# Performance work log

Measured on AMD Instinct MI355X. Metric: run time of the kernel, lower is better.

Reference implementation:

```python
import jax, jax.numpy as jnp
import numpy as np

H = 256; NH = 8; DH = H // NH; L = 2; B = 32; S = 512; FIN = 199; A = 4


def _ln(x, g, b):
    m = jnp.mean(x, -1, keepdims=True)
    v = jnp.mean((x - m) ** 2, -1, keepdims=True)
    return (x - m) / jnp.sqrt(v + 1e-5) * g + b


def _grn(x, fc1w, fc1b, fc2w, fc2b, gw, gb, ggw, ggb, lg, lb):
    # GatedResidualNetwork, input_dim == output_dim so no skip layer, no context
    h = jax.nn.elu(x @ fc1w + fc1b)
    h = jax.nn.elu(h @ fc2w + fc2b)
    g = (h @ gw + gb) * jax.nn.sigmoid(h @ ggw + ggb)  # GLU
    return _ln(g + x, lg, lb)


def _attn(h, wq, bq, wk, bk, wv, bv, wo, bo):
    b, s, _ = h.shape
    q = (h @ wq + bq).reshape(b, s, NH, DH)
    k = (h @ wk + bk).reshape(b, s, NH, DH)
    v = (h @ wv + bv).reshape(b, s, NH, DH)
    scores = jnp.einsum('bqhd,bkhd->bhqk', q, k) / jnp.sqrt(jnp.float32(DH))
    mask = jnp.triu(jnp.ones((s, s), dtype=bool), 1)  # causal: mask strictly-future
    scores = jnp.where(mask, -jnp.inf, scores)
    aw = jax.nn.softmax(scores, axis=-1)
    ctx = jnp.einsum('bhqk,bkhd->bqhd', aw, v).reshape(b, s, H)
    return ctx @ wo + bo, aw


def _pe(s, d):
    pos = jnp.arange(s, dtype=jnp.float32)[:, None]
    div = jnp.exp(jnp.arange(0, d, 2, dtype=jnp.float32) * (-jnp.log(10000.0) / d))
    pe = jnp.zeros((s, d), dtype=jnp.float32)
    pe = pe.at[:, 0::2].set(jnp.sin(pos * div)).at[:, 1::2].set(jnp.cos(pos * div))
    return pe


def setup_inputs():
    key = jax.random.key(0)
    ks = iter(jax.random.split(key, 80))
    def nrm(shape, sc=0.02):
        return (jax.random.normal(next(ks), shape) * sc).astype(jnp.float32)
    d = {}
    d['x'] = jax.random.normal(next(ks), (B, S, FIN), dtype=jnp.float32)
    d['time_features'] = jax.random.normal(next(ks), (B, S, 3), dtype=jnp.float32)
    d['fp_w'] = nrm((FIN, H)); d['fp_b'] = jnp.zeros((H,), jnp.float32)
    d['tp_w'] = nrm((3, H));   d['tp_b'] = jnp.zeros((H,), jnp.float32)
    d['ip_w'] = nrm((H, H));   d['ip_b'] = jnp.zeros((H,), jnp.float32)
    for nm in ['wq', 'wk', 'wv', 'wo']:
        d[nm] = nrm((L, H, H))
    for nm in ['bq', 'bk', 'bv', 'bo']:
        d[nm] = jnp.zeros((L, H), jnp.float32)
    d['ln_g'] = jnp.ones((L, H), jnp.float32); d['ln_b'] = jnp.zeros((L, H), jnp.float32)
    for nm in ['g_fc1w', 'g_fc2w', 'g_gw', 'g_ggw']:
        d[nm] = nrm((L, H, H))
    for nm in ['g_fc1b', 'g_fc2b', 'g_gb', 'g_ggb']:
        d[nm] = jnp.zeros((L, H), jnp.float32)
    d['g_lg'] = jnp.ones((L, H), jnp.float32); d['g_lb'] = jnp.zeros((L, H), jnp.float32)
    for nm in ['f_fc1w', 'f_fc2w', 'f_gw', 'f_ggw']:
        d[nm] = nrm((H, H))
    for nm in ['f_fc1b', 'f_fc2b', 'f_gb', 'f_ggb']:
        d[nm] = jnp.zeros((H,), jnp.float32)
    d['f_lg'] = jnp.ones((H,), jnp.float32); d['f_lb'] = jnp.zeros((H,), jnp.float32)
    d['out_w'] = nrm((H, A)); d['out_b'] = jnp.zeros((A,), jnp.float32)
    return d


def reference(x, time_features, fp_w, fp_b, tp_w, tp_b, ip_w, ip_b,
              wq, bq, wk, bk, wv, bv, wo, bo, ln_g, ln_b,
              g_fc1w, g_fc1b, g_fc2w, g_fc2b, g_gw, g_gb, g_ggw, g_ggb, g_lg, g_lb,
              f_fc1w, f_fc1b, f_fc2w, f_fc2b, f_gw, f_gb, f_ggw, f_ggb, f_lg, f_lb,
              out_w, out_b):
    s = x.shape[1]
    hidden = (x @ fp_w + fp_b) + (time_features @ tp_w + tp_b)
    hidden = hidden @ ip_w + ip_b
    hidden = hidden + _pe(s, H)[None]
    aw = None
    for i in range(L):
        ao, aw = _attn(hidden, wq[i], bq[i], wk[i], bk[i], wv[i], bv[i], wo[i], bo[i])
        hidden = _ln(hidden + ao, ln_g[i], ln_b[i])
        hidden = _grn(hidden, g_fc1w[i], g_fc1b[i], g_fc2w[i], g_fc2b[i],
                      g_gw[i], g_gb[i], g_ggw[i], g_ggb[i], g_lg[i], g_lb[i])
    hidden = _grn(hidden, f_fc1w, f_fc1b, f_fc2w, f_fc2b, f_gw, f_gb, f_ggw, f_ggb, f_lg, f_lb)
    final = hidden[:, -1, :]
    logits = final @ out_w + out_b  # [B, A], one column per target asset
    return (logits, aw)
```

## Files before the change

kernel.cpp:

```cpp
#include <hip/hip_runtime.h>
#include <math.h>
#include <cstddef>

#define H 256
#define NH 8
#define DH 32
#define LAYERS 2
#define BB 32
#define SS 512
#define FINDIM 199
#define AA 4
#define T_TOK (BB*SS)

typedef unsigned short u16;
typedef unsigned int u32;
typedef __attribute__((ext_vector_type(8))) short short8;
typedef __attribute__((ext_vector_type(4))) float f4;

__device__ __forceinline__ float b2f(u16 v){
  unsigned u = ((unsigned)v) << 16;
  return __builtin_bit_cast(float, u);
}
__device__ __forceinline__ u16 f2b(float f){
  unsigned u = __builtin_bit_cast(unsigned, f);
  unsigned r = (u + 0x7fffu + ((u >> 16) & 1u)) >> 16;
  return (u16)r;
}
__device__ __forceinline__ float wave_sum(float v){
  #pragma unroll
  for (int mk=1; mk<64; mk<<=1) v += __shfl_xor(v, mk, 64);
  return v;
}

#define GLD_LDS16(g, l) \
  __builtin_amdgcn_global_load_lds((const __attribute__((address_space(1))) void*)(g), \
                                   (__attribute__((address_space(3))) void*)(l), 16, 0, 0)

struct WPtrs { const float* p[21]; };

__global__ __launch_bounds__(256) void wconv_kernel(WPtrs wp, u16* __restrict__ dst){
  __shared__ float tl[64][65];
  int mb = blockIdx.x >> 4, tile = blockIdx.x & 15;
  int k0 = (tile >> 2) * 64, n0 = (tile & 3) * 64;
  const float* src = wp.p[mb];
  int t = threadIdx.x;
  int r = t >> 4, cg = t & 15;
  #pragma unroll
  for (int p4=0;p4<4;p4++){
    f4 v = *(const f4*)(src + (size_t)(k0 + r + p4*16)*H + n0 + cg*4);
    tl[r+p4*16][cg*4+0]=v[0]; tl[r+p4*16][cg*4+1]=v[1];
    tl[r+p4*16][cg*4+2]=v[2]; tl[r+p4*16][cg*4+3]=v[3];
  }
  __syncthreads();
  u16* db = dst + (size_t)mb*H*H;
  #pragma unroll
  for (int p4=0;p4<4;p4++){
    int rn = r + p4*16;
    ushort4 o;
    o.x = f2b(tl[cg*4+0][rn]); o.y = f2b(tl[cg*4+1][rn]);
    o.z = f2b(tl[cg*4+2][rn]); o.w = f2b(tl[cg*4+3][rn]);
    *(ushort4*)(db + (size_t)(n0+rn)*H + k0 + cg*4) = o;
  }
}

__global__ __launch_bounds__(256) void in_proj_kernel(
    const float* __restrict__ x, const float* __restrict__ tf,
    const float* __restrict__ fp_w, const float* __restrict__ fp_b,
    const float* __restrict__ tp_w, const float* __restrict__ tp_b,
    u16* __restrict__ out) {
  __shared__ float xs[8][FINDIM];
  __shared__ float ts[8][3];
  int t = threadIdx.x;
  int tok0 = blockIdx.x * 8;
  for (int idx = t; idx < 8*FINDIM; idx += 256) {
    int r = idx / FINDIM, k = idx % FINDIM;
    xs[r][k] = x[(size_t)(tok0+r)*FINDIM + k];
  }
  if (t < 24) { int r = t/3, k = t%3; ts[r][k] = tf[(size_t)(tok0+r)*3 + k]; }
  __syncthreads();
  int c = t;
  float base = fp_b[c] + tp_b[c];
  float acc[8];
  #pragma unroll
  for (int r=0;r<8;r++) acc[r] = base;
  for (int k=0;k<FINDIM;k++){
    float w = fp_w[k*H + c];
    #pragma unroll
    for (int r=0;r<8;r++) acc[r] = fmaf(xs[r][k], w, acc[r]);
  }
  #pragma unroll
  for (int k=0;k<3;k++){
    float w = tp_w[k*H + c];
    #pragma unroll
    for (int r=0;r<8;r++) acc[r] = fmaf(ts[r][k], w, acc[r]);
  }
  #pragma unroll
  for (int r=0;r<8;r++) out[(size_t)(tok0+r)*H + c] = f2b(acc[r]);
}

struct GemmJob  { const u16* Wt; const float* bias; u16* C; };
struct GemmBatch{ GemmJob j[3]; };

template<int EPI>
__global__ __launch_bounds__(256) void gemm_bf16(
    const u16* __restrict__ A, GemmBatch jb) {
  __shared__ u16 smem[128*64 + 64*64];
  u16* As  = smem;
  u16* Wsm = smem + 128*64;
  const GemmJob job = jb.j[blockIdx.z];
  const u16* Wt = job.Wt;
  int t = threadIdx.x;
  int m0 = blockIdx.x * 128;
  int n0 = blockIdx.y * 64;
  int lane = t & 63, w = t >> 6;
  int wr = (w >> 1) * 64;
  int wc = (w & 1) * 32;
  int l16 = lane & 15, lq = lane >> 4;

  f4 acc[4][2];
  #pragma unroll
  for (int mi=0;mi<4;mi++)
    #pragma unroll
    for (int ni=0;ni<2;ni++) acc[mi][ni] = (f4){0.f,0.f,0.f,0.f};

  for (int k0=0;k0<256;k0+=64){
    #pragma unroll
    for (int ja=0;ja<4;ja++){
      int ub = (w*4 + ja)*64;
      int u  = ub + lane;
      int m  = u >> 3, c = u & 7, kx = c ^ (m & 7);
      const u16* g = A + (size_t)(m0+m)*H + k0 + kx*8;
      GLD_LDS16(g, As + (size_t)ub*8);
    }
    #pragma unroll
    for (int jb2=0;jb2<2;jb2++){
      int ub = (w*2 + jb2)*64;
      int u  = ub + lane;
      int n  = u >> 3, c = u & 7, kx = c ^ (n & 7);
      const u16* g = Wt + (size_t)(n0+n)*H + k0 + kx*8;
      GLD_LDS16(g, Wsm + (size_t)ub*8);
    }
    __syncthreads();
    #pragma unroll
    for (int kc=0;kc<2;kc++){
      short8 af[4], bf[2];
      int kx = kc*4 + lq;
      #pragma unroll
      for (int mi=0;mi<4;mi++){
        int m = wr + mi*16 + l16;
        int un = (m<<3) | (kx ^ (m&7));
        af[mi] = *(short8*)&As[un*8];
      }
      #pragma unroll
      for (int ni=0;ni<2;ni++){
        int n = wc + ni*16 + l16;
        int un = (n<<3) | (kx ^ (n&7));
        bf[ni] = *(short8*)&Wsm[un*8];
      }
      #pragma unroll
      for (int mi=0;mi<4;mi++)
        #pragma unroll
        for (int ni=0;ni<2;ni++)
          acc[mi][ni] = __builtin_amdgcn_mfma_f32_16x16x32_bf16(af[mi], bf[ni], acc[mi][ni], 0,0,0);
    }
    __syncthreads();
  }

  u16* Cl = smem;
  #pragma unroll
  for (int ni=0;ni<2;ni++){
    int coll = wc + ni*16 + l16;
    float bcol = job.bias[n0 + coll];
    #pragma unroll
    for (int mi=0;mi<4;mi++){
      #pragma unroll
      for (int r=0;r<4;r++){
        int rowl = wr + mi*16 + lq*4 + r;
        float v = acc[mi][ni][r] + bcol;
        if (EPI==1) v = v > 0.f ? v : expm1f(v);
        if (EPI==2) {
          int s  = (m0 + rowl) & (SS-1);
          int ii = (n0 + coll) >> 1;
          float div = __expf((float)(2*ii) * -0.03597789207803197f);
          float arg = (float)s * div;
          v += ((n0+coll) & 1) ? cosf(arg) : sinf(arg);
        }
        Cl[rowl*68 + coll] = f2b(v);
      }
    }
  }
  __syncthreads();
  #pragma unroll
  for (int q2=0;q2<4;q2++){
    int u = q2*256 + t;
    int row = u >> 3, cu = u & 7;
    short8 val = *(short8*)&Cl[row*68 + cu*8];
    *(short8*)(job.C + (size_t)(m0+row)*H + n0 + cu*8) = val;
  }
}

template<int WRITE_AW>
__global__ __launch_bounds__(256) void attn_kernel(
    const u16* __restrict__ q, const u16* __restrict__ k,
    const u16* __restrict__ v, float* __restrict__ aw,
    u16* __restrict__ ctx) {
  __shared__ u16 Vt[DH][SS+8];
  __shared__ u16 Plds[4][16][72];
  int t  = threadIdx.x;
  int zg = blockIdx.x;
  int bh = blockIdx.y;
  int b  = bh >> 3, h = bh & 7;
  int lane = t & 63, w = t >> 6;
  int l16 = lane & 15, lq = lane >> 4;
  const float scale = 0.17677669529663687f;

  #pragma unroll
  for (int rep=0;rep<2;rep++){
    int kk = t + rep*256;
    const u16* vp = v + ((size_t)(b*SS + kk))*H + h*DH;
    short8 r0 = *(const short8*)(vp);
    short8 r1 = *(const short8*)(vp+8);
    short8 r2 = *(const short8*)(vp+16);
    short8 r3 = *(const short8*)(vp+24);
    #pragma unroll
    for (int j=0;j<8;j++){
      Vt[j][kk]    = (u16)r0[j];
      Vt[8+j][kk]  = (u16)r1[j];
      Vt[16+j][kk] = (u16)r2[j];
      Vt[24+j][kk] = (u16)r3[j];
    }
  }
  __syncthreads();

  for (int it=0; it<4; it++){
    int qt  = zg + it*2;
    int qr0 = qt*64 + w*16;
    int KT  = qt*4 + w + 1;
    short8 af = *(const short8*)(q + ((size_t)(b*SS + qr0 + l16))*H + h*DH + lq*8);

    float l[4] = {0.f,0.f,0.f,0.f};
    f4 o[2] = {(f4){0.f,0.f,0.f,0.f}, (f4){0.f,0.f,0.f,0.f}};
    u32 pk0[32], pk1[32];

    #pragma unroll
    for (int c8=0;c8<8;c8++){
      if (c8*4 < KT){
        #pragma unroll
        for (int j=0;j<4;j++){
          int kt = c8*4 + j;
          float p[4] = {0.f,0.f,0.f,0.f};
          if (kt < KT){
            short8 bfr = *(const short8*)(k + ((size_t)(b*SS + kt*16 + l16))*H + h*DH + lq*8);
            f4 cc = (f4){0.f,0.f,0.f,0.f};
            cc = __builtin_amdgcn_mfma_f32_16x16x32_bf16(af, bfr, cc, 0,0,0);
            int col = kt*16 + l16;
            #pragma unroll
            for (int i=0;i<4;i++){
              int qi = qr0 + lq*4 + i;
              float sc = (col <= qi) ? cc[i]*scale : -3.0e38f;
              p[i] = __expf(sc);
              l[i] += p[i];
            }
          }
          u16 pb[4];
          #pragma unroll
          for (int i=0;i<4;i++) pb[i] = f2b(p[i]);
          if (WRITE_AW){
            pk0[kt] = (u32)pb[0] | ((u32)pb[1] << 16);
            pk1[kt] = (u32)pb[2] | ((u32)pb[3] << 16);
          }
          #pragma unroll
          for (int i=0;i<4;i++) Plds[w][lq*4+i][j*16+l16] = pb[i];
        }
        #pragma unroll
        for (int kc=0;kc<2;kc++){
          short8 pa = *(short8*)&Plds[w][l16][kc*32 + lq*8];
          #pragma unroll
          for (int dt=0;dt<2;dt++){
            short8 vb = *(const short8*)&Vt[dt*16 + l16][c8*64 + kc*32 + lq*8];
            o[dt] = __builtin_amdgcn_mfma_f32_16x16x32_bf16(pa, vb, o[dt], 0,0,0);
          }
        }
      }
    }

    #pragma unroll
    for (int i=0;i<4;i++){
      #pragma unroll
      for (int mk=1; mk<16; mk<<=1) l[i] += __shfl_xor(l[i], mk, 64);
    }
    float inv[4];
    #pragma unroll
    for (int i=0;i<4;i++) inv[i] = 1.0f / l[i];

    if (WRITE_AW){
      float* ab = aw + (size_t)bh*SS*SS;
      #pragma unroll
      for (int kt=0;kt<32;kt++){
        if (kt < KT){
          int col = kt*16 + l16;
          float pv[4] = { b2f((u16)pk0[kt]), b2f((u16)(pk0[kt]>>16)),
                          b2f((u16)pk1[kt]), b2f((u16)(pk1[kt]>>16)) };
          #pragma unroll
          for (int i=0;i<4;i++){
            int qi = qr0 + lq*4 + i;
            ab[(size_t)qi*SS + col] = (col <= qi) ? pv[i]*inv[i] : 0.f;
          }
        }
      }
      int c4base = KT*4;
      f4 z = (f4){0.f,0.f,0.f,0.f};
      #pragma unroll
      for (int ri=0;ri<4;ri++){
        int row = qr0 + ri*4 + lq;
        for (int j=l16; j < 128 - c4base; j += 16)
          *(f4*)&ab[(size_t)row*SS + (size_t)(c4base+j)*4] = z;
      }
    }

    #pragma unroll
    for (int dt=0;dt<2;dt++){
      #pragma unroll
      for (int i=0;i<4;i++){
        int row = qr0 + lq*4 + i;
        ctx[((size_t)(b*SS + row))*H + h*DH + dt*16 + l16] = f2b(o[dt][i]*inv[i]);
      }
    }
  }
}

__global__ __launch_bounds__(256) void add_ln_kernel(
    u16* __restrict__ hid, const u16* __restrict__ ao,
    const float* __restrict__ g, const float* __restrict__ b){
  int wv = threadIdx.x>>6, lane = threadIdx.x&63;
  size_t tok = (size_t)blockIdx.x*4 + wv;
  u16* hp = hid + tok*H + lane*4;
  ushort4 h4 = *(ushort4*)hp;
  ushort4 a4 = *(const ushort4*)(ao + tok*H + lane*4);
  float xv[4] = {b2f(h4.x)+b2f(a4.x), b2f(h4.y)+b2f(a4.y),
                 b2f(h4.z)+b2f(a4.z), b2f(h4.w)+b2f(a4.w)};
  float s=0.f, ss=0.f;
  #pragma unroll
  for (int j=0;j<4;j++){ s += xv[j]; ss += xv[j]*xv[j]; }
  s = wave_sum(s); ss = wave_sum(ss);
  float mean = s * (1.0f/H);
  float var  = ss * (1.0f/H) - mean*mean;
  float rstd = rsqrtf(var + 1e-5f);
  ushort4 o;
  int col = lane*4;
  o.x = f2b((xv[0]-mean)*rstd*g[col+0] + b[col+0]);
  o.y = f2b((xv[1]-mean)*rstd*g[col+1] + b[col+1]);
  o.z = f2b((xv[2]-mean)*rstd*g[col+2] + b[col+2]);
  o.w = f2b((xv[3]-mean)*rstd*g[col+3] + b[col+3]);
  *(ushort4*)hp = o;
}

__global__ __launch_bounds__(256) void gate_ln_kernel(
    const u16* __restrict__ gbuf, const u16* __restrict__ ggbuf,
    u16* __restrict__ hid,
    const float* __restrict__ lg, const float* __restrict__ lb){
  int wv = threadIdx.x>>6, lane = threadIdx.x&63;
  size_t tok = (size_t)blockIdx.x*4 + wv;
  u16* hp = hid + tok*H + lane*4;
  ushort4 g4  = *(const ushort4*)(gbuf  + tok*H + lane*4);
  ushort4 gg4 = *(const ushort4*)(ggbuf + tok*H + lane*4);
  ushort4 h4  = *(ushort4*)hp;
  float gv[4]  = {b2f(g4.x),  b2f(g4.y),  b2f(g4.z),  b2f(g4.w)};
  float ggv[4] = {b2f(gg4.x), b2f(gg4.y), b2f(gg4.z), b2f(gg4.w)};
  float hv[4]  = {b2f(h4.x),  b2f(h4.y),  b2f(h4.z),  b2f(h4.w)};
  float xv[4];
  #pragma unroll
  for (int j=0;j<4;j++){
    float sg = 1.0f/(1.0f + __expf(-ggv[j]));
    xv[j] = gv[j]*sg + hv[j];
  }
  float s=0.f, ss=0.f;
  #pragma unroll
  for (int j=0;j<4;j++){ s += xv[j]; ss += xv[j]*xv[j]; }
  s = wave_sum(s); ss = wave_sum(ss);
  float mean = s * (1.0f/H);
  float var  = ss * (1.0f/H) - mean*mean;
  float rstd = rsqrtf(var + 1e-5f);
  ushort4 o;
  int col = lane*4;
  o.x = f2b((xv[0]-mean)*rstd*lg[col+0] + lb[col+0]);
  o.y = f2b((xv[1]-mean)*rstd*lg[col+1] + lb[col+1]);
  o.z = f2b((xv[2]-mean)*rstd*lg[col+2] + lb[col+2]);
  o.w = f2b((xv[3]-mean)*rstd*lg[col+3] + lb[col+3]);
  *(ushort4*)hp = o;
}

__global__ __launch_bounds__(128) void logits_kernel(
    const u16* __restrict__ hid, const float* __restrict__ ow,
    const float* __restrict__ ob, float* __restrict__ out){
  int t = threadIdx.x;
  int b = t >> 2, a = t & 3;
  const u16* hr = hid + ((size_t)b*SS + (SS-1))*H;
  float acc = ob[a];
  for (int k2=0;k2<H;k2++) acc = fmaf(b2f(hr[k2]), ow[k2*AA + a], acc);
  out[t] = acc;
}

extern "C" void kernel_launch(void* const* d_in, const int* in_sizes, int n_in,
                              void* d_out, int out_size, void* d_ws, size_t ws_size,
                              hipStream_t stream){
  (void)in_sizes; (void)n_in; (void)out_size; (void)ws_size;
  const float* x      = (const float*)d_in[0];
  const float* tf     = (const float*)d_in[1];
  const float* fp_w   = (const float*)d_in[2];
  const float* fp_b   = (const float*)d_in[3];
  const float* tp_w   = (const float*)d_in[4];
  const float* tp_b   = (const float*)d_in[5];
  const float* ip_w   = (const float*)d_in[6];
  const float* ip_b   = (const float*)d_in[7];
  const float* wq     = (const float*)d_in[8];
  const float* wk     = (const float*)d_in[9];
  const float* wv     = (const float*)d_in[10];
  const float* wo     = (const float*)d_in[11];
  const float* bq     = (const float*)d_in[12];
  const float* bk     = (const float*)d_in[13];
  const float* bv     = (const float*)d_in[14];
  const float* bo     = (const float*)d_in[15];
  const float* ln_g   = (const float*)d_in[16];
  const float* ln_b   = (const float*)d_in[17];
  const float* g_fc1w = (const float*)d_in[18];
  const float* g_fc2w = (const float*)d_in[19];
  const float* g_gw   = (const float*)d_in[20];
  const float* g_ggw  = (const float*)d_in[21];
  const float* g_fc1b = (const float*)d_in[22];
  const float* g_fc2b = (const float*)d_in[23];
  const float* g_gb   = (const float*)d_in[24];
  const float* g_ggb  = (const float*)d_in[25];
  const float* g_lg   = (const float*)d_in[26];
  const float* g_lb   = (const float*)d_in[27];
  const float* f_fc1w = (const float*)d_in[28];
  const float* f_fc2w = (const float*)d_in[29];
  const float* f_gw   = (const float*)d_in[30];
  const float* f_ggw  = (const float*)d_in[31];
  const float* f_fc1b = (const float*)d_in[32];
  const float* f_fc2b = (const float*)d_in[33];
  const float* f_gb   = (const float*)d_in[34];
  const float* f_ggb  = (const float*)d_in[35];
  const float* f_lg   = (const float*)d_in[36];
  const float* f_lb   = (const float*)d_in[37];
  const float* out_w  = (const float*)d_in[38];
  const float* out_b  = (const float*)d_in[39];

  float* logits = (float*)d_out;
  float* aw     = logits + BB*AA;

  u16* wts = (u16*)d_ws;
  const size_t WMAT = (size_t)H*H;
  u16* hid  = wts  + 21*WMAT;
  size_t BUF = (size_t)T_TOK * H;
  u16* buf1 = hid  + BUF;
  u16* buf2 = buf1 + BUF;
  u16* buf3 = buf2 + BUF;

  WPtrs wp;
  wp.p[0]  = ip_w;
  wp.p[1]  = wq;        wp.p[2]  = wq + WMAT;
  wp.p[3]  = wk;        wp.p[4]  = wk + WMAT;
  wp.p[5]  = wv;        wp.p[6]  = wv + WMAT;
  wp.p[7]  = wo;        wp.p[8]  = wo + WMAT;
  wp.p[9]  = g_fc1w;    wp.p[10] = g_fc1w + WMAT;
  wp.p[11] = g_fc2w;    wp.p[12] = g_fc2w + WMAT;
  wp.p[13] = g_gw;      wp.p[14] = g_gw + WMAT;
  wp.p[15] = g_ggw;     wp.p[16] = g_ggw + WMAT;
  wp.p[17] = f_fc1w;    wp.p[18] = f_fc2w;
  wp.p[19] = f_gw;      wp.p[20] = f_ggw;
  const int WT_IP=0, WT_Q=1, WT_K=3, WT_V=5, WT_O=7,
            WT_FC1=9, WT_FC2=11, WT_GW=13, WT_GGW=15,
            WT_FFC1=17, WT_FFC2=18, WT_FGW=19, WT_FGGW=20;

  dim3 b256(256);
  dim3 gAttn(2, BB*NH);

  auto mkbatch = [&](int w0, const float* b0, u16* c0,
                     int w1, const float* b1, u16* c1,
                     int w2, const float* b2, u16* c2) {
    GemmBatch gb;
    gb.j[0] = { wts + (size_t)w0*WMAT, b0, c0 };
    gb.j[1] = { wts + (size_t)(w1<0?w0:w1)*WMAT, (w1<0?b0:b1), (w1<0?c0:c1) };
    gb.j[2] = { wts + (size_t)(w2<0?w0:w2)*WMAT, (w2<0?b0:b2), (w2<0?c0:c2) };
    return gb;
  };

  wconv_kernel<<<21*16, b256, 0, stream>>>(wp, wts);
  in_proj_kernel<<<T_TOK/8, b256, 0, stream>>>(x, tf, fp_w, fp_b, tp_w, tp_b, buf1);

  gemm_bf16<2><<<dim3(T_TOK/128, H/64, 1), b256, 0, stream>>>(
      buf1, mkbatch(WT_IP, ip_b, hid, -1,0,0, -1,0,0));

  for (int i=0;i<LAYERS;i++){
    const size_t BOFF = (size_t)i*H;
    gemm_bf16<0><<<dim3(T_TOK/128, H/64, 3), b256, 0, stream>>>(
        hid, mkbatch(WT_Q+i, bq+BOFF, buf1, WT_K+i, bk+BOFF, buf2, WT_V+i, bv+BOFF, buf3));
    if (i == LAYERS-1)
      attn_kernel<1><<<gAttn, b256, 0, stream>>>(buf1, buf2, buf3, aw, buf1);
    else
      attn_kernel<0><<<gAttn, b256, 0, stream>>>(buf1, buf2, buf3, aw, buf1);
    gemm_bf16<0><<<dim3(T_TOK/128, H/64, 1), b256, 0, stream>>>(
        buf1, mkbatch(WT_O+i, bo+BOFF, buf2, -1,0,0, -1,0,0));
    add_ln_kernel<<<T_TOK/4, b256, 0, stream>>>(hid, buf2, ln_g + BOFF, ln_b + BOFF);
    gemm_bf16<1><<<dim3(T_TOK/128, H/64, 1), b256, 0, stream>>>(
        hid, mkbatch(WT_FC1+i, g_fc1b+BOFF, buf1, -1,0,0, -1,0,0));
    gemm_bf16<1><<<dim3(T_TOK/128, H/64, 1), b256, 0, stream>>>(
        buf1, mkbatch(WT_FC2+i, g_fc2b+BOFF, buf2, -1,0,0, -1,0,0));
    gemm_bf16<0><<<dim3(T_TOK/128, H/64, 2), b256, 0, stream>>>(
        buf2, mkbatch(WT_GW+i, g_gb+BOFF, buf3, WT_GGW+i, g_ggb+BOFF, buf1, -1,0,0));
    gate_ln_kernel<<<T_TOK/4, b256, 0, stream>>>(buf3, buf1, hid, g_lg + BOFF, g_lb + BOFF);
  }

  gemm_bf16<1><<<dim3(T_TOK/128, H/64, 1), b256, 0, stream>>>(
      hid, mkbatch(WT_FFC1, f_fc1b, buf1, -1,0,0, -1,0,0));
  gemm_bf16<1><<<dim3(T_TOK/128, H/64, 1), b256, 0, stream>>>(
      buf1, mkbatch(WT_FFC2, f_fc2b, buf2, -1,0,0, -1,0,0));
  gemm_bf16<0><<<dim3(T_TOK/128, H/64, 2), b256, 0, stream>>>(
      buf2, mkbatch(WT_FGW, f_gb, buf3, WT_FGGW, f_ggb, buf1, -1,0,0));
  gate_ln_kernel<<<T_TOK/4, b256, 0, stream>>>(buf3, buf1, hid, f_lg, f_lb);

  logits_kernel<<<1, 128, 0, stream>>>(hid, out_w, out_b, logits);
}
```

Baseline: 748.5 us.

## Fuse GRN, O-projection+LN and input projection into per-token-tile MFMA kernels

Replaces the chain of separate GEMM and layernorm kernels with fused kernels. Each block holds a 32-token tile in LDS and runs the successive 256x256 matmuls with MFMA, keeping intermediates on chip: the O-projection with residual and layernorm, the whole GRN (fc1, fc2, GLU, residual, LN), and the input projection done as a bf16 MFMA GEMM over padded concatenated features followed by ip_w and positional encoding. This removes several global round-trips of the activation buffers and many launches. In exchange, B fragments are read straight from global memory (L2) without LDS staging or double buffering, there are only 512 blocks, and an extra padded bf16 copy of the input is materialised.

```diff
diff --git a/kernel.cpp b/kernel.cpp
--- a/kernel.cpp
+++ b/kernel.cpp
@@ -11,6 +11,7 @@
 #define FINDIM 199
 #define AA 4
 #define T_TOK (BB*SS)
+#define KIN 224
 
 typedef unsigned short u16;
 typedef unsigned int u32;
@@ -35,6 +36,89 @@
 #define GLD_LDS16(g, l) \
   __builtin_amdgcn_global_load_lds((const __attribute__((address_space(1))) void*)(g), \
                                    (__attribute__((address_space(3))) void*)(l), 16, 0, 0)
+
+template<int KC, int WK>
+__device__ __forceinline__ void stage_acc(
+    const u16* Xl, int sx, const u16* __restrict__ Wt,
+    int c0, int l16, int lq, f4 acc[2][2])
+{
+  #pragma unroll
+  for (int mi=0;mi<2;mi++)
+    #pragma unroll
+    for (int ni=0;ni<2;ni++) acc[mi][ni] = (f4){0.f,0.f,0.f,0.f};
+  #pragma unroll
+  for (int kc=0;kc<KC;kc++){
+    short8 af[2], bf[2];
+    af[0] = *(const short8*)&Xl[(l16)*sx      + kc*32 + lq*8];
+    af[1] = *(const short8*)&Xl[(16+l16)*sx   + kc*32 + lq*8];
+    bf[0] = *(const short8*)(Wt + (size_t)(c0+l16)*WK    + kc*32 + lq*8);
+    bf[1] = *(const short8*)(Wt + (size_t)(c0+16+l16)*WK + kc*32 + lq*8);
+    #pragma unroll
+    for (int mi=0;mi<2;mi++)
+      #pragma unroll
+      for (int ni=0;ni<2;ni++)
+        acc[mi][ni] = __builtin_amdgcn_mfma_f32_16x16x32_bf16(af[mi], bf[ni], acc[mi][ni], 0,0,0);
+  }
+}
+
+template<int DO_ELU>
+__device__ __forceinline__ void stage_store(
+    f4 acc[2][2], const float* __restrict__ bias,
+    int c0, int l16, int lq, u16* Yl, int sy)
+{
+  #pragma unroll
+  for (int ni=0;ni<2;ni++){
+    int col = c0 + ni*16 + l16;
+    float bc = bias[col];
+    #pragma unroll
+    for (int mi=0;mi<2;mi++){
+      #pragma unroll
+      for (int r=0;r<4;r++){
+        int row = mi*16 + lq*4 + r;
+        float v = acc[mi][ni][r] + bc;
+        if (DO_ELU) v = v > 0.f ? v : expm1f(v);
+        Yl[row*sy + col] = f2b(v);
+      }
+    }
+  }
+}
+
+__device__ __forceinline__ void tile_load256(const u16* g, u16* Yl, int sy, int t){
+  #pragma unroll
+  for (int j=0;j<2;j++){
+    int u = t + j*512;
+    int row = u >> 5, cu = u & 31;
+    *(short8*)&Yl[row*sy + cu*8] = *(const short8*)(g + (size_t)row*H + cu*8);
+  }
+}
+
+__device__ __forceinline__ void tile_ln(
+    const u16* Yl, int sy, const float* __restrict__ g, const float* __restrict__ b,
+    u16* out, int t)
+{
+  int w = t >> 6, lane = t & 63;
+  #pragma unroll
+  for (int rr=0;rr<4;rr++){
+    int row = w*4 + rr;
+    float xv[4];
+    #pragma unroll
+    for (int j=0;j<4;j++) xv[j] = b2f(Yl[row*sy + lane*4 + j]);
+    float s=0.f, ss=0.f;
+    #pragma unroll
+    for (int j=0;j<4;j++){ s += xv[j]; ss += xv[j]*xv[j]; }
+    s = wave_sum(s); ss = wave_sum(ss);
+    float mean = s * (1.0f/H);
+    float var  = ss * (1.0f/H) - mean*mean;
+    float rstd = rsqrtf(var + 1e-5f);
+    ushort4 o;
+    int col = lane*4;
+    o.x = f2b((xv[0]-mean)*rstd*g[col+0] + b[col+0]);
+    o.y = f2b((xv[1]-mean)*rstd*g[col+1] + b[col+1]);
+    o.z = f2b((xv[2]-mean)*rstd*g[col+2] + b[col+2]);
+    o.w = f2b((xv[3]-mean)*rstd*g[col+3] + b[col+3]);
+    *(ushort4*)(out + (size_t)row*H + col) = o;
+  }
+}
 
 struct WPtrs { const float* p[21]; };
 
@@ -63,45 +147,183 @@
   }
 }
 
-__global__ __launch_bounds__(256) void in_proj_kernel(
+__global__ __launch_bounds__(256) void wcat_kernel(
+    const float* __restrict__ fp_w, const float* __restrict__ tp_w,
+    u16* __restrict__ wcat){
+  int idx = blockIdx.x*256 + threadIdx.x;
+  if (idx >= 256*KIN) return;
+  int n = idx / KIN, k2 = idx % KIN;
+  float v = 0.f;
+  if (k2 < FINDIM) v = fp_w[(size_t)k2*H + n];
+  else if (k2 < FINDIM+3) v = tp_w[(size_t)(k2-FINDIM)*H + n];
+  wcat[idx] = f2b(v);
+}
+
+__global__ __launch_bounds__(256) void xconv_kernel(
     const float* __restrict__ x, const float* __restrict__ tf,
-    const float* __restrict__ fp_w, const float* __restrict__ fp_b,
-    const float* __restrict__ tp_w, const float* __restrict__ tp_b,
-    u16* __restrict__ out) {
-  __shared__ float xs[8][FINDIM];
-  __shared__ float ts[8][3];
+    u16* __restrict__ ab){
+  size_t idx = (size_t)blockIdx.x*256 + threadIdx.x;
+  if (idx >= (size_t)T_TOK*KIN) return;
+  int tok = idx / KIN, k2 = idx % KIN;
+  float v = 0.f;
+  if (k2 < FINDIM) v = x[(size_t)tok*FINDIM + k2];
+  else if (k2 < FINDIM+3) v = tf[(size_t)tok*3 + (k2-FINDIM)];
+  ab[idx] = f2b(v);
+}
+
+#define SA (KIN+8)
+#define SY (H+8)
+
+__global__ __launch_bounds__(512) void input_kernel(
+    const u16* __restrict__ ab, const u16* __restrict__ wcat,
+    const float* __restrict__ fp_b, const float* __restrict__ tp_b,
+    const u16* __restrict__ ipw, const float* __restrict__ ip_b,
+    u16* __restrict__ hid){
+  __shared__ u16 Al[32*SA];
+  __shared__ u16 Tl[32*SY];
   int t = threadIdx.x;
-  int tok0 = blockIdx.x * 8;
-  for (int idx = t; idx < 8*FINDIM; idx += 256) {
-    int r = idx / FINDIM, k = idx % FINDIM;
-    xs[r][k] = x[(size_t)(tok0+r)*FINDIM + k];
-  }
-  if (t < 24) { int r = t/3, k = t%3; ts[r][k] = tf[(size_t)(tok0+r)*3 + k]; }
-  __syncthreads();
-  int c = t;
-  float base = fp_b[c] + tp_b[c];
-  float acc[8];
-  #pragma unroll
-  for (int r=0;r<8;r++) acc[r] = base;
-  for (int k=0;k<FINDIM;k++){
-    float w = fp_w[k*H + c];
-    #pragma unroll
-    for (int r=0;r<8;r++) acc[r] = fmaf(xs[r][k], w, acc[r]);
-  }
-  #pragma unroll
-  for (int k=0;k<3;k++){
-    float w = tp_w[k*H + c];
-    #pragma unroll
-    for (int r=0;r<8;r++) acc[r] = fmaf(ts[r][k], w, acc[r]);
-  }
-  #pragma unroll
-  for (int r=0;r<8;r++) out[(size_t)(tok0+r)*H + c] = f2b(acc[r]);
+  int tok0 = blockIdx.x * 32;
+  int lane = t & 63, w = t >> 6;
+  int l16 = lane & 15, lq = lane >> 4;
+  int c0 = w * 32;
+
+  #pragma unroll
+  for (int j=0;j<2;j++){
+    int u = t + j*512;
+    if (u < 896){
+      int row = u / 28, cu = u % 28;
+      *(short8*)&Al[row*SA + cu*8] = *(const short8*)(ab + (size_t)(tok0+row)*KIN + cu*8);
+    }
+  }
+  __syncthreads();
+
+  f4 acc[2][2];
+  stage_acc<7, KIN>(Al, SA, wcat, c0, l16, lq, acc);
+  #pragma unroll
+  for (int ni=0;ni<2;ni++){
+    int col = c0 + ni*16 + l16;
+    float bc = fp_b[col] + tp_b[col];
+    #pragma unroll
+    for (int mi=0;mi<2;mi++)
+      #pragma unroll
+      for (int r=0;r<4;r++){
+        int row = mi*16 + lq*4 + r;
+        Tl[row*SY + col] = f2b(acc[mi][ni][r] + bc);
+      }
+  }
+  __syncthreads();
+
+  stage_acc<8, H>(Tl, SY, ipw, c0, l16, lq, acc);
+  #pragma unroll
+  for (int ni=0;ni<2;ni++){
+    int col = c0 + ni*16 + l16;
+    float bc = ip_b[col];
+    int ii = col >> 1;
+    float div = __expf((float)(2*ii) * -0.03597789207803197f);
+    #pragma unroll
+    for (int mi=0;mi<2;mi++)
+      #pragma unroll
+      for (int r=0;r<4;r++){
+        int row = mi*16 + lq*4 + r;
+        int s = (tok0 + row) & (SS-1);
+        float arg = (float)s * div;
+        float pe = (col & 1) ? cosf(arg) : sinf(arg);
+        hid[(size_t)(tok0+row)*H + col] = f2b(acc[mi][ni][r] + bc + pe);
+      }
+  }
+}
+
+__global__ __launch_bounds__(512) void oproj_ln_kernel(
+    const u16* __restrict__ ctx, u16* __restrict__ hid,
+    const u16* __restrict__ wo, const float* __restrict__ bo,
+    const float* __restrict__ g, const float* __restrict__ b){
+  __shared__ u16 Xl[32*SY];
+  __shared__ u16 Rl[32*SY];
+  int t = threadIdx.x;
+  int tok0 = blockIdx.x * 32;
+  int lane = t & 63, w = t >> 6;
+  int l16 = lane & 15, lq = lane >> 4;
+  int c0 = w * 32;
+  u16* hb = hid + (size_t)tok0*H;
+
+  tile_load256(ctx + (size_t)tok0*H, Xl, SY, t);
+  tile_load256(hb, Rl, SY, t);
+  __syncthreads();
+
+  f4 acc[2][2];
+  stage_acc<8, H>(Xl, SY, wo, c0, l16, lq, acc);
+  __syncthreads();
+  #pragma unroll
+  for (int ni=0;ni<2;ni++){
+    int col = c0 + ni*16 + l16;
+    float bc = bo[col];
+    #pragma unroll
+    for (int mi=0;mi<2;mi++)
+      #pragma unroll
+      for (int r=0;r<4;r++){
+        int row = mi*16 + lq*4 + r;
+        float y = acc[mi][ni][r] + bc + b2f(Rl[row*SY + col]);
+        Xl[row*SY + col] = f2b(y);
+      }
+  }
+  __syncthreads();
+  tile_ln(Xl, SY, g, b, hb, t);
+}
+
+__global__ __launch_bounds__(512) void grn_kernel(
+    u16* __restrict__ hid,
+    const u16* __restrict__ fc1, const u16* __restrict__ fc2,
+    const u16* __restrict__ gw,  const u16* __restrict__ ggw,
+    const float* __restrict__ b1, const float* __restrict__ b2,
+    const float* __restrict__ gb, const float* __restrict__ ggb,
+    const float* __restrict__ lg, const float* __restrict__ lb){
+  __shared__ u16 Xl[32*SY];
+  __shared__ u16 H1[32*SY];
+  __shared__ u16 H2[32*SY];
+  int t = threadIdx.x;
+  int tok0 = blockIdx.x * 32;
+  int lane = t & 63, w = t >> 6;
+  int l16 = lane & 15, lq = lane >> 4;
+  int c0 = w * 32;
+  u16* hb = hid + (size_t)tok0*H;
+
+  tile_load256(hb, Xl, SY, t);
+  __syncthreads();
+
+  f4 acc[2][2];
+  stage_acc<8, H>(Xl, SY, fc1, c0, l16, lq, acc);
+  stage_store<1>(acc, b1, c0, l16, lq, H1, SY);
+  __syncthreads();
+  stage_acc<8, H>(H1, SY, fc2, c0, l16, lq, acc);
+  stage_store<1>(acc, b2, c0, l16, lq, H2, SY);
+  __syncthreads();
+  stage_acc<8, H>(H2, SY, gw, c0, l16, lq, acc);
+  stage_store<0>(acc, gb, c0, l16, lq, H1, SY);
+  __syncthreads();
+  stage_acc<8, H>(H2, SY, ggw, c0, l16, lq, acc);
+  __syncthreads();
+  #pragma unroll
+  for (int ni=0;ni<2;ni++){
+    int col = c0 + ni*16 + l16;
+    float bc = ggb[col];
+    #pragma unroll
+    for (int mi=0;mi<2;mi++)
+      #pragma unroll
+      for (int r=0;r<4;r++){
+        int row = mi*16 + lq*4 + r;
+        float gg = acc[mi][ni][r] + bc;
+        float sg = 1.0f/(1.0f + __expf(-gg));
+        float y  = b2f(H1[row*SY + col]) * sg + b2f(Xl[row*SY + col]);
+        H2[row*SY + col] = f2b(y);
+      }
+  }
+  __syncthreads();
+  tile_ln(H2, SY, lg, lb, hb, t);
 }
 
 struct GemmJob  { const u16* Wt; const float* bias; u16* C; };
 struct GemmBatch{ GemmJob j[3]; };
 
-template<int EPI>
 __global__ __launch_bounds__(256) void gemm_bf16(
     const u16* __restrict__ A, GemmBatch jb) {
   __shared__ u16 smem[128*64 + 64*64];
@@ -176,16 +398,7 @@
       #pragma unroll
       for (int r=0;r<4;r++){
         int rowl = wr + mi*16 + lq*4 + r;
-        float v = acc[mi][ni][r] + bcol;
-        if (EPI==1) v = v > 0.f ? v : expm1f(v);
-        if (EPI==2) {
-          int s  = (m0 + rowl) & (SS-1);
-          int ii = (n0 + coll) >> 1;
-          float div = __expf((float)(2*ii) * -0.03597789207803197f);
-          float arg = (float)s * div;
-          v += ((n0+coll) & 1) ? cosf(arg) : sinf(arg);
-        }
-        Cl[rowl*68 + coll] = f2b(v);
+        Cl[rowl*68 + coll] = f2b(acc[mi][ni][r] + bcol);
       }
     }
   }
@@ -327,67 +540,6 @@
       }
     }
   }
-}
-
-__global__ __launch_bounds__(256) void add_ln_kernel(
-    u16* __restrict__ hid, const u16* __restrict__ ao,
-    const float* __restrict__ g, const float* __restrict__ b){
-  int wv = threadIdx.x>>6, lane = threadIdx.x&63;
-  size_t tok = (size_t)blockIdx.x*4 + wv;
-  u16* hp = hid + tok*H + lane*4;
-  ushort4 h4 = *(ushort4*)hp;
-  ushort4 a4 = *(const ushort4*)(ao + tok*H + lane*4);
-  float xv[4] = {b2f(h4.x)+b2f(a4.x), b2f(h4.y)+b2f(a4.y),
-                 b2f(h4.z)+b2f(a4.z), b2f(h4.w)+b2f(a4.w)};
-  float s=0.f, ss=0.f;
-  #pragma unroll
-  for (int j=0;j<4;j++){ s += xv[j]; ss += xv[j]*xv[j]; }
-  s = wave_sum(s); ss = wave_sum(ss);
-  float mean = s * (1.0f/H);
-  float var  = ss * (1.0f/H) - mean*mean;
-  float rstd = rsqrtf(var + 1e-5f);
-  ushort4 o;
-  int col = lane*4;
-  o.x = f2b((xv[0]-mean)*rstd*g[col+0] + b[col+0]);
-  o.y = f2b((xv[1]-mean)*rstd*g[col+1] + b[col+1]);
-  o.z = f2b((xv[2]-mean)*rstd*g[col+2] + b[col+2]);
-  o.w = f2b((xv[3]-mean)*rstd*g[col+3] + b[col+3]);
-  *(ushort4*)hp = o;
-}
-
-__global__ __launch_bounds__(256) void gate_ln_kernel(
-    const u16* __restrict__ gbuf, const u16* __restrict__ ggbuf,
-    u16* __restrict__ hid,
-    const float* __restrict__ lg, const float* __restrict__ lb){
-  int wv = threadIdx.x>>6, lane = threadIdx.x&63;
-  size_t tok = (size_t)blockIdx.x*4 + wv;
-  u16* hp = hid + tok*H + lane*4;
-  ushort4 g4  = *(const ushort4*)(gbuf  + tok*H + lane*4);
-  ushort4 gg4 = *(const ushort4*)(ggbuf + tok*H + lane*4);
-  ushort4 h4  = *(ushort4*)hp;
-  float gv[4]  = {b2f(g4.x),  b2f(g4.y),  b2f(g4.z),  b2f(g4.w)};
-  float ggv[4] = {b2f(gg4.x), b2f(gg4.y), b2f(gg4.z), b2f(gg4.w)};
-  float hv[4]  = {b2f(h4.x),  b2f(h4.y),  b2f(h4.z),  b2f(h4.w)};
-  float xv[4];
-  #pragma unroll
-  for (int j=0;j<4;j++){
-    float sg = 1.0f/(1.0f + __expf(-ggv[j]));
-    xv[j] = gv[j]*sg + hv[j];
-  }
-  float s=0.f, ss=0.f;
-  #pragma unroll
-  for (int j=0;j<4;j++){ s += xv[j]; ss += xv[j]*xv[j]; }
-  s = wave_sum(s); ss = wave_sum(ss);
-  float mean = s * (1.0f/H);
-  float var  = ss * (1.0f/H) - mean*mean;
-  float rstd = rsqrtf(var + 1e-5f);
-  ushort4 o;
-  int col = lane*4;
-  o.x = f2b((xv[0]-mean)*rstd*lg[col+0] + lb[col+0]);
-  o.y = f2b((xv[1]-mean)*rstd*lg[col+1] + lb[col+1]);
-  o.z = f2b((xv[2]-mean)*rstd*lg[col+2] + lb[col+2]);
-  o.w = f2b((xv[3]-mean)*rstd*lg[col+3] + lb[col+3]);
-  *(ushort4*)hp = o;
 }
 
 __global__ __launch_bounds__(128) void logits_kernel(
@@ -451,7 +603,9 @@
 
   u16* wts = (u16*)d_ws;
   const size_t WMAT = (size_t)H*H;
-  u16* hid  = wts  + 21*WMAT;
+  u16* wcat = wts  + 21*WMAT;
+  u16* abuf = wcat + (size_t)H*KIN;
+  u16* hid  = abuf + (size_t)T_TOK*KIN;
   size_t BUF = (size_t)T_TOK * H;
   u16* buf1 = hid  + BUF;
   u16* buf2 = buf1 + BUF;
@@ -473,52 +627,40 @@
             WT_FC1=9, WT_FC2=11, WT_GW=13, WT_GGW=15,
             WT_FFC1=17, WT_FFC2=18, WT_FGW=19, WT_FGGW=20;
 
-  dim3 b256(256);
+  dim3 b256(256), b512(512);
   dim3 gAttn(2, BB*NH);
-
-  auto mkbatch = [&](int w0, const float* b0, u16* c0,
-                     int w1, const float* b1, u16* c1,
-                     int w2, const float* b2, u16* c2) {
-    GemmBatch gb;
-    gb.j[0] = { wts + (size_t)w0*WMAT, b0, c0 };
-    gb.j[1] = { wts + (size_t)(w1<0?w0:w1)*WMAT, (w1<0?b0:b1), (w1<0?c0:c1) };
-    gb.j[2] = { wts + (size_t)(w2<0?w0:w2)*WMAT, (w2<0?b0:b2), (w2<0?c0:c2) };
-    return gb;
-  };
+  dim3 gTok(T_TOK/32);
 
   wconv_kernel<<<21*16, b256, 0, stream>>>(wp, wts);
-  in_proj_kernel<<<T_TOK/8, b256, 0, stream>>>(x, tf, fp_w, fp_b, tp_w, tp_b, buf1);
-
-  gemm_bf16<2><<<dim3(T_TOK/128, H/64, 1), b256, 0, stream>>>(
-      buf1, mkbatch(WT_IP, ip_b, hid, -1,0,0, -1,0,0));
+  wcat_kernel<<<(H*KIN+255)/256, b256, 0, stream>>>(fp_w, tp_w, wcat);
+  xconv_kernel<<<(T_TOK*KIN+255)/256, b256, 0, stream>>>(x, tf, abuf);
+  input_kernel<<<gTok, b512, 0, stream>>>(abuf, wcat, fp_b, tp_b,
+                                          wts + (size_t)WT_IP*WMAT, ip_b, hid);
 
   for (int i=0;i<LAYERS;i++){
     const size_t BOFF = (size_t)i*H;
-    gemm_bf16<0><<<dim3(T_TOK/128, H/64, 3), b256, 0, stream>>>(
-        hid, mkbatch(WT_Q+i, bq+BOFF, buf1, WT_K+i, bk+BOFF, buf2, WT_V+i, bv+BOFF, buf3));
+    GemmBatch gb;
+    gb.j[0] = { wts + (size_t)(WT_Q+i)*WMAT, bq+BOFF, buf1 };
+    gb.j[1] = { wts + (size_t)(WT_K+i)*WMAT, bk+BOFF, buf2 };
+    gb.j[2] = { wts + (size_t)(WT_V+i)*WMAT, bv+BOFF, buf3 };
+    gemm_bf16<<<dim3(T_TOK/128, H/64, 3), b256, 0, stream>>>(hid, gb);
     if (i == LAYERS-1)
       attn_kernel<1><<<gAttn, b256, 0, stream>>>(buf1, buf2, buf3, aw, buf1);
     else
       attn_kernel<0><<<gAttn, b256, 0, stream>>>(buf1, buf2, buf3, aw, buf1);
-    gemm_bf16<0><<<dim3(T_TOK/128, H/64, 1), b256, 0, stream>>>(
-        buf1, mkbatch(WT_O+i, bo+BOFF, buf2, -1,0,0, -1,0,0));
-    add_ln_kernel<<<T_TOK/4, b256, 0, stream>>>(hid, buf2, ln_g + BOFF, ln_b + BOFF);
-    gemm_bf16<1><<<dim3(T_TOK/128, H/64, 1), b256, 0, stream>>>(
-        hid, mkbatch(WT_FC1+i, g_fc1b+BOFF, buf1, -1,0,0, -1,0,0));
-    gemm_bf16<1><<<dim3(T_TOK/128, H/64, 1), b256, 0, stream>>>(
-        buf1, mkbatch(WT_FC2+i, g_fc2b+BOFF, buf2, -1,0,0, -1,0,0));
-    gemm_bf16<0><<<dim3(T_TOK/128, H/64, 2), b256, 0, stream>>>(
-        buf2, mkbatch(WT_GW+i, g_gb+BOFF, buf3, WT_GGW+i, g_ggb+BOFF, buf1, -1,0,0));
-    gate_ln_kernel<<<T_TOK/4, b256, 0, stream>>>(buf3, buf1, hid, g_lg + BOFF, g_lb + BOFF);
-  }
-
-  gemm_bf16<1><<<dim3(T_TOK/128, H/64, 1), b256, 0, stream>>>(
-      hid, mkbatch(WT_FFC1, f_fc1b, buf1, -1,0,0, -1,0,0));
-  gemm_bf16<1><<<dim3(T_TOK/128, H/64, 1), b256, 0, stream>>>(
-      buf1, mkbatch(WT_FFC2, f_fc2b, buf2, -1,0,0, -1,0,0));
-  gemm_bf16<0><<<dim3(T_TOK/128, H/64, 2), b256, 0, stream>>>(
-      buf2, mkbatch(WT_FGW, f_gb, buf3, WT_FGGW, f_ggb, buf1, -1,0,0));
-  gate_ln_kernel<<<T_TOK/4, b256, 0, stream>>>(buf3, buf1, hid, f_lg, f_lb);
+    oproj_ln_kernel<<<gTok, b512, 0, stream>>>(buf1, hid,
+        wts + (size_t)(WT_O+i)*WMAT, bo+BOFF, ln_g+BOFF, ln_b+BOFF);
+    grn_kernel<<<gTok, b512, 0, stream>>>(hid,
+        wts + (size_t)(WT_FC1+i)*WMAT, wts + (size_t)(WT_FC2+i)*WMAT,
+        wts + (size_t)(WT_GW+i)*WMAT,  wts + (size_t)(WT_GGW+i)*WMAT,
+        g_fc1b+BOFF, g_fc2b+BOFF, g_gb+BOFF, g_ggb+BOFF,
+        g_lg+BOFF, g_lb+BOFF);
+  }
+
+  grn_kernel<<<gTok, b512, 0, stream>>>(hid,
+      wts + (size_t)WT_FFC1*WMAT, wts + (size_t)WT_FFC2*WMAT,
+      wts + (size_t)WT_FGW*WMAT,  wts + (size_t)WT_FGGW*WMAT,
+      f_fc1b, f_fc2b, f_gb, f_ggb, f_lg, f_lb);
 
   logits_kernel<<<1, 128, 0, stream>>>(hid, out_w, out_b, logits);
 }
```

Measured after the change: 673.6 us. 1.11x faster.
